# Kernel tuning notes

Hardware: AMD Instinct MI355X
Metric: run time of the kernel (lower is better)

The kernel has to match this reference:

```python
import jax, jax.numpy as jnp
import numpy as np
import math

B, CIN, COUT, K, G, SD, H = 8, 512, 512, 3, 16, 512, 32
EPS = 1e-8


def _blur_kernel():
    k = jnp.array([1., 3., 3., 1.], dtype=jnp.float32)
    k = k[None, :] * k[:, None]
    k = k / k.sum()
    return k * 4.0  # upsample_factor ** 2


def setup_inputs() -> dict:
    key = jax.random.key(0)
    ks = jax.random.split(key, 10)
    return {
        "x": jax.random.normal(ks[0], (B, CIN, H, H), jnp.float32),
        "co": jax.random.uniform(ks[1], (1, CIN, CIN), jnp.float32),
        "style": jax.random.normal(ks[2], (B, 2 * SD), jnp.float32),
        "noise": jax.random.normal(ks[3], (B, 1, 2 * H, 2 * H), jnp.float32),
        "W": jax.random.normal(ks[4], (1, COUT, CIN, K, K), jnp.float32),
        "mb_w": jax.random.normal(ks[5], (G, SD), jnp.float32),
        "mb_b": jnp.ones((G,), jnp.float32),
        "mod_w": jax.random.normal(ks[6], (CIN, SD), jnp.float32),
        "mod_b": jnp.ones((CIN,), jnp.float32),
        "cluster": jax.random.normal(ks[7], (G, CIN), jnp.float32),
        "gate": -jnp.ones((1,), jnp.float32),
        "tmpr": -2.0 * jnp.ones((1,), jnp.float32),
        "noise_weight": jnp.zeros((1,), jnp.float32),
        "flr_bias": jnp.zeros((COUT,), jnp.float32),
    }


def _l2norm(x, axis):
    n = jnp.linalg.norm(x, axis=axis, keepdims=True)
    return x / jnp.maximum(n, 1e-12)


def reference(x, co, style, noise, W, mb_w, mb_b, mod_w, mod_b,
              cluster, gate, tmpr, noise_weight, flr_bias):
    scale = 1.0 / math.sqrt(CIN * K * K)   # GroupModulatedConv2d.scale
    lin_scale = 1.0 / math.sqrt(SD)        # EqualLinear scale (lr_mul=1)

    t = jax.nn.sigmoid(tmpr) * 5.0
    g = jax.nn.sigmoid(gate)
    S = jax.nn.sigmoid((co - g) * 50.0)                    # (1,Cin,Cin)
    cl = jax.nn.softmax(t * cluster, axis=0)               # (G,Cin)
    loss1 = jnp.sum((cl.T @ cl - jax.lax.stop_gradient(S)) ** 2)
    loss2 = jnp.sum((jnp.float32(CIN * CIN / G) - jnp.sum(S)) ** 2)
    grouped = jax.lax.stop_gradient(jnp.round(jax.nn.softmax(cl * 500.0, axis=0))) + 1e-6

    s1, s2 = style[:, :SD], style[:, SD:]
    style_base = (s1 @ (mb_w * lin_scale).T + mb_b)[:, :, None]   # (B,G,1)
    st = (s2 @ (mod_w * lin_scale).T + mod_b)[:, None, :]         # (B,1,Cin)
    tmp = _l2norm(grouped[None] * st, axis=2)                     # (B,G,Cin)
    st = jnp.sum(tmp * style_base, axis=1)                        # (B,Cin)

    w = scale * W * st[:, None, :, None, None]                    # (B,Cout,Cin,K,K)
    demod = jax.lax.rsqrt(jnp.sum(w * w, axis=(2, 3, 4)) + EPS)   # (B,Cout)
    w = w * demod[:, :, None, None, None]

    # conv_transpose2d(stride=2, pad=0, groups=B) == per-sample conv with
    # lhs_dilation=2, padding=K-1, spatially-flipped kernel.
    wf = w[:, :, :, ::-1, ::-1]

    def per_sample(xi, wi):  # xi (Cin,h,w), wi (Cout,Cin,K,K)
        return jax.lax.conv_general_dilated(
            xi[None], wi, window_strides=(1, 1),
            padding=((K - 1, K - 1), (K - 1, K - 1)), lhs_dilation=(2, 2),
            dimension_numbers=('NCHW', 'OIHW', 'NCHW'))[0]

    out = jax.vmap(per_sample)(x, wf)                             # (B,Cout,65,65)

    # Blur: upfirdn2d, pad=(1,1), depthwise 4x4 symmetric FIR kernel.
    bk = _blur_kernel()
    kdw = jnp.broadcast_to(bk[None, None], (COUT, 1, 4, 4))
    out = jax.lax.conv_general_dilated(
        out, kdw, (1, 1), ((1, 1), (1, 1)), feature_group_count=COUT,
        dimension_numbers=('NCHW', 'OIHW', 'NCHW'))                # (B,Cout,64,64)

    # Correlation of base weights (detached, fed to next layer as `co`).
    wflat = W.reshape(COUT, -1)
    wn = _l2norm(wflat, axis=1)
    co_out = jax.lax.stop_gradient((wn @ wn.T)[None])              # (1,Cout,Cout)

    # NoiseInjection + FusedLeakyReLU
    out = out + noise_weight * noise
    out = jax.nn.leaky_relu(out + flr_bias[None, :, None, None], 0.2) * math.sqrt(2.0)
    return out, co_out, loss1, loss2
```

## Files before the change

kernel.cpp:

```cpp
#include <hip/hip_runtime.h>
#include <hip/hip_bf16.h>

#define NB 8
#define LIN_SCALE 0.044194173824159216f
#define SCALE 0.014731391274719736f

typedef __attribute__((ext_vector_type(8))) short short8;
typedef __attribute__((ext_vector_type(4))) float floatx4;

static constexpr size_t O_XS   = 0;
static constexpr size_t O_OUT1 = 9469952;
static constexpr size_t O_WRT  = 44081152;
static constexpr size_t O_WB   = 48799744;
static constexpr size_t O_PG   = 53518336;
static constexpr size_t O_WSQ  = 61906944;
static constexpr size_t O_CL   = 62955520;
static constexpr size_t O_GR   = O_CL + 32768;
static constexpr size_t O_SB   = O_GR + 32768;
static constexpr size_t O_ST0  = O_SB + 1024;
static constexpr size_t O_STS  = O_ST0 + 16384;
static constexpr size_t O_ST2  = O_STS + 16384;
static constexpr size_t O_WNI  = O_ST2 + 16384;
static constexpr size_t O_DM   = O_WNI + 2048;
static constexpr size_t O_ACC  = O_DM + 16384;

static constexpr size_t OUT_CO = 16777216;
static constexpr size_t OUT_L  = 17039360;

__device__ const int c_ylim[4] = {33,33,32,32};
__device__ const int c_xlim[4] = {33,32,33,32};
__device__ const int c_ntap[4] = {4,2,2,1};
__device__ const int c_tap0[4] = {0,4,6,8};
__device__ const int c_nmb[4]  = {69,66,66,64};
__device__ const int c_cnt[4]  = {276,264,264,256};
__device__ const int c_dy[9] = {-1,-1,0,0, -1,0, 0,0, 0};
__device__ const int c_dx[9] = {-1,0,-1,0, 0,0, -1,0, 0};
__device__ const int c_ky[9] = {2,2,0,0, 2,0, 1,1, 1};
__device__ const int c_kx[9] = {2,0,2,0, 1,1, 2,0, 1};
__device__ const long c_poff[4] = {0, 4460544, 8785920, 13111296};

__device__ __forceinline__ float wave_red(float v) {
#pragma unroll
  for (int s = 32; s > 0; s >>= 1) v += __shfl_down(v, s);
  return v;
}

__device__ __forceinline__ void gl_lds16(const void* g, void* l) {
  __builtin_amdgcn_global_load_lds((const __attribute__((address_space(1))) void*)g,
                                   (__attribute__((address_space(3))) void*)l, 16, 0, 0);
}

__device__ __forceinline__ unsigned short bf16b(float f) {
  union { __hip_bfloat16 h; unsigned short u; } cv;
  cv.h = __float2bfloat16(f);
  return cv.u;
}

__device__ __forceinline__ float bfu(unsigned short u) {
  union { float f; unsigned u32; } c; c.u32 = ((unsigned)u) << 16; return c.f;
}

__device__ __forceinline__ int xcd_chunk(int lb, int cnt) {
  const int q = cnt >> 3, r = cnt & 7;
  const int c = lb & 7, i = lb >> 3;
  return (c < r) ? c*(q+1) + i : r*(q+1) + (c - r)*q + i;
}

__global__ __launch_bounds__(256) void k_big1(const float* __restrict__ W,
    float* __restrict__ wsq, float* __restrict__ wni,
    __hip_bfloat16* __restrict__ wrt, unsigned short* __restrict__ wb,
    const float* __restrict__ style, const float* __restrict__ mod_w,
    const float* __restrict__ mod_b, float* __restrict__ st0,
    const float* __restrict__ co, const float* __restrict__ gate,
    const float* __restrict__ cluster, const float* __restrict__ tmpr,
    const float* __restrict__ mb_w, const float* __restrict__ mb_b,
    float* __restrict__ gr, float* __restrict__ sb,
    float* __restrict__ pacc, __hip_bfloat16* __restrict__ xs) {
  __shared__ float sh[8192];
  __shared__ float extra[8];
  const int bid = blockIdx.x, tid = threadIdx.x;
  const int lane = tid & 63, wv = tid >> 6;
  if (bid < 512) {
    const int o = bid;
    for (int j = tid; j < 4608; j += 256) sh[j] = W[(size_t)o*4608 + j];
    __syncthreads();
    float tot = 0.f;
#pragma unroll
    for (int half = 0; half < 2; half++) {
      const int i = tid + half*256;
      float s = 0.f;
#pragma unroll
      for (int k = 0; k < 9; k++) { float w = sh[i*9 + k]; s = fmaf(w, w, s); }
      wsq[o*512 + i] = s; tot += s;
#pragma unroll
      for (int tp = 0; tp < 9; tp++)
        wrt[((size_t)tp*512 + o)*512 + i] = __float2bfloat16(sh[i*9 + c_ky[tp]*3 + c_kx[tp]]);
    }
    for (int j = tid; j < 4608; j += 256) wb[(size_t)o*4608 + j] = bf16b(sh[j]);
    tot = wave_red(tot);
    if (lane == 0) extra[wv] = tot;
    __syncthreads();
    if (tid == 0) wni[o] = 1.f / fmaxf(sqrtf(extra[0]+extra[1]+extra[2]+extra[3]), 1e-12f);
  } else if (bid < 576) {
    const int b = (bid - 512) >> 3, oc = (bid - 512) & 7;
    sh[tid] = style[b*1024 + 512 + tid];
    sh[tid + 256] = style[b*1024 + 768 + tid];
    __syncthreads();
#pragma unroll
    for (int rr = 0; rr < 16; rr++) {
      const int c = oc*64 + wv*16 + rr;
      const float* mw = mod_w + (size_t)c*512;
      float acc = 0.f;
#pragma unroll
      for (int it = 0; it < 8; it++) acc = fmaf(mw[lane + 64*it], sh[lane + 64*it], acc);
      acc = wave_red(acc);
      if (lane == 0) st0[b*512 + c] = acc*LIN_SCALE + mod_b[c];
    }
  } else if (bid < 1088) {
    const int i = bid - 576;
    const float tt = 5.f / (1.f + expf(-tmpr[0]));
    const float gg = 1.f / (1.f + expf(-gate[0]));
    for (int j = tid; j < 512; j += 256) {
      float v[16]; float m = -1e30f;
#pragma unroll
      for (int g = 0; g < 16; g++) { v[g] = tt * cluster[g*512 + j]; m = fmaxf(m, v[g]); }
      float s = 0.f;
#pragma unroll
      for (int g = 0; g < 16; g++) { v[g] = expf(v[g] - m); s += v[g]; }
      float inv = 1.f / s;
#pragma unroll
      for (int g = 0; g < 16; g++) sh[g*512 + j] = v[g] * inv;
    }
    __syncthreads();
    float cli[16];
#pragma unroll
    for (int k = 0; k < 16; k++) cli[k] = sh[k*512 + i];
    float p1 = 0.f, p2 = 0.f;
    for (int j = tid; j < 512; j += 256) {
      float d = 0.f;
#pragma unroll
      for (int k = 0; k < 16; k++) d = fmaf(cli[k], sh[k*512 + j], d);
      float S = 1.f / (1.f + expf(-50.f*(co[i*512 + j] - gg)));
      float e = d - S;
      p1 = fmaf(e, e, p1); p2 += S;
    }
    p1 = wave_red(p1); p2 = wave_red(p2);
    if (lane == 0) { extra[wv] = p1; extra[4 + wv] = p2; }
    __syncthreads();
    if (tid == 0)  pacc[i]       = extra[0]+extra[1]+extra[2]+extra[3];
    if (tid == 64) pacc[512 + i] = extra[4]+extra[5]+extra[6]+extra[7];
  } else if (bid == 1088) {
    const float tt = 5.f / (1.f + expf(-tmpr[0]));
#pragma unroll
    for (int h = 0; h < 2; h++) {
      const int c = tid + h*256;
      float v[16]; float m = -1e30f;
#pragma unroll
      for (int g = 0; g < 16; g++) { v[g] = tt * cluster[g*512 + c]; m = fmaxf(m, v[g]); }
      float s = 0.f;
#pragma unroll
      for (int g = 0; g < 16; g++) { v[g] = expf(v[g] - m); s += v[g]; }
      float inv = 1.f / s;
      float clv[16]; float m2 = -1e30f;
#pragma unroll
      for (int g = 0; g < 16; g++) { clv[g] = v[g]*inv; m2 = fmaxf(m2, 500.f*clv[g]); }
      float s2 = 0.f; float e2[16];
#pragma unroll
      for (int g = 0; g < 16; g++) { e2[g] = expf(500.f*clv[g] - m2); s2 += e2[g]; }
      float i2 = 1.f / s2;
#pragma unroll
      for (int g = 0; g < 16; g++) gr[g*512 + c] = rintf(e2[g]*i2) + 1e-6f;
    }
    for (int task = wv; task < 128; task += 4) {
      int b = task >> 4, g = task & 15;
      const float* s1 = style + b*1024;
      const float* mw = mb_w + g*512;
      float acc = 0.f;
#pragma unroll
      for (int it = 0; it < 8; it++) acc = fmaf(s1[lane + 64*it], mw[lane + 64*it], acc);
      acc = wave_red(acc);
      if (lane == 0) sb[b*16 + g] = acc*LIN_SCALE + mb_b[g];
    }
  } else {
    const int id0 = (bid - 1089)*256 + tid;
    const float4 z = make_float4(0.f, 0.f, 0.f, 0.f);
    float4* xq = (float4*)xs;
#pragma unroll
    for (int it = 0; it < 22; ++it) {
      const int id = id0 + it*3072;
      const int c = id & 63;
      const int pb = id >> 6;
      const int b = pb / 132;
      const int pix = pb - b*132;
      int y, xx;
      if (pix < 34)       { y = 0;        xx = pix; }
      else if (pix < 68)  { y = 33;       xx = pix - 34; }
      else if (pix < 100) { y = pix - 67; xx = 0; }
      else                { y = pix - 99; xx = 33; }
      xq[((size_t)(b*34 + y)*34 + xx)*64 + c] = z;
    }
  }
}

__global__ __launch_bounds__(256) void k_mix(const float* __restrict__ st0,
    const float* __restrict__ gr, const float* __restrict__ sb,
    float* __restrict__ sts, float* __restrict__ st2,
    const float* __restrict__ pacc, float* __restrict__ out_tail) {
  if (blockIdx.x == 8) {
    const int tid = threadIdx.x;
    const int lane = tid & 63, wv = tid >> 6;
    __shared__ float r1[4], r2[4];
    float a = pacc[tid] + pacc[tid + 256];
    float b = pacc[512 + tid] + pacc[768 + tid];
    a = wave_red(a); b = wave_red(b);
    if (lane == 0) { r1[wv] = a; r2[wv] = b; }
    __syncthreads();
    if (tid == 0) {
      float p1 = r1[0]+r1[1]+r1[2]+r1[3];
      float p2 = r2[0]+r2[1]+r2[2]+r2[3];
      out_tail[0] = p1;
      float d = 16384.f - p2;
      out_tail[1] = d*d;
    }
    return;
  }
  const int b = blockIdx.x, tid = threadIdx.x;
  const int lane = tid & 63, wv = tid >> 6;
  float s0 = st0[b*512 + tid], s1 = st0[b*512 + 256 + tid];
  float g0[16], g1[16];
#pragma unroll
  for (int g = 0; g < 16; g++) { g0[g] = gr[g*512 + tid]; g1[g] = gr[g*512 + 256 + tid]; }
  __shared__ float red[16][4];
  __shared__ float inv[16];
  __shared__ float sbb[16];
#pragma unroll
  for (int g = 0; g < 16; g++) {
    float a = g0[g]*s0, c = g1[g]*s1;
    float p = wave_red(a*a + c*c);
    if (lane == 0) red[g][wv] = p;
  }
  if (tid < 16) sbb[tid] = sb[b*16 + tid];
  __syncthreads();
  if (tid < 16) {
    float tt = red[tid][0] + red[tid][1] + red[tid][2] + red[tid][3];
    inv[tid] = 1.f / fmaxf(sqrtf(tt), 1e-12f);
  }
  __syncthreads();
  float f0 = 0.f, f1 = 0.f;
#pragma unroll
  for (int g = 0; g < 16; g++) {
    float w = inv[g]*sbb[g];
    f0 = fmaf(g0[g], w, f0); f1 = fmaf(g1[g], w, f1);
  }
  float sn0 = s0*f0, sn1 = s1*f1;
  sts[b*512 + tid] = sn0*SCALE;        st2[b*512 + tid] = sn0*sn0;
  sts[b*512 + 256 + tid] = sn1*SCALE;  st2[b*512 + 256 + tid] = sn1*sn1;
}

__global__ __launch_bounds__(256) void k_big2(const float* __restrict__ st2,
    const float* __restrict__ wsq, float* __restrict__ dm,
    const float* __restrict__ x, const float* __restrict__ sts,
    __hip_bfloat16* __restrict__ xs) {
  __shared__ float L[64*65];
  const int tid = threadIdx.x;
  const int lane = tid & 63, wv = tid >> 6;
  if (blockIdx.x < 64) {
    const int b = blockIdx.x >> 3, oc = blockIdx.x & 7;
    L[tid] = st2[b*512 + tid];
    L[tid + 256] = st2[b*512 + 256 + tid];
    __syncthreads();
#pragma unroll
    for (int rr = 0; rr < 16; rr++) {
      const int o = oc*64 + wv*16 + rr;
      const float* wp = wsq + (size_t)o*512;
      float acc = 0.f;
#pragma unroll
      for (int it = 0; it < 8; it++) acc = fmaf(wp[lane + 64*it], L[lane + 64*it], acc);
      acc = wave_red(acc);
      if (lane == 0) dm[b*512 + o] = rsqrtf((1.0f/4608.0f)*acc + 1e-8f);
    }
    return;
  }
  const int id = blockIdx.x - 64;
  const int b = id >> 7;
  const int p0 = ((id >> 3) & 15) * 64;
  const int i0 = (id & 7) * 64;
  const int lp = tid & 63, li = tid >> 6;
  const float* xp = x + ((size_t)b*512 + i0)*1024 + p0;
#pragma unroll
  for (int ii = 0; ii < 16; ii++) {
    const int i = li + 4*ii;
    L[i*65 + lp] = xp[(size_t)i*1024 + lp];
  }
  __syncthreads();
  const int iw = tid & 63, pw = tid >> 6;
  const float sv = sts[b*512 + i0 + iw];
#pragma unroll
  for (int pp = 0; pp < 16; pp++) {
    const int pix = p0 + pw + 4*pp;
    const int y = pix >> 5, xq = pix & 31;
    xs[(((size_t)b*34 + (y+1))*34 + (xq+1))*512 + i0 + iw] = __float2bfloat16(L[iw*65 + pw + 4*pp] * sv);
  }
}

__global__ __launch_bounds__(256, 4) void k_mfma(
    const __hip_bfloat16* __restrict__ xs, const __hip_bfloat16* __restrict__ wrt,
    __hip_bfloat16* __restrict__ out1, const __hip_bfloat16* __restrict__ wb,
    float* __restrict__ pgram) {
  __shared__ __hip_bfloat16 smem[8704];
  const int fid = blockIdx.x;
  const int tid = threadIdx.x;
  const int lane = tid & 63, wv = tid >> 6;
  const int wm = (wv >> 1) << 6, wn = (wv & 1) << 6;
  const int col16 = lane & 15, quad = lane >> 4;
  const int colp = col16 ^ ((col16 >> 2) & 1);
  const int soff = (quad ^ (col16 & 3)) << 3;

  int aoff[4], boff[4];
#pragma unroll
  for (int t = 0; t < 4; t++) {
    aoff[t] = (wm + t*16 + colp)*32 + soff;
    boff[t] = 4096 + (wn + t*16 + colp)*32 + soff;
  }
  floatx4 acc[4][4];
#pragma unroll
  for (int i = 0; i < 4; i++)
#pragma unroll
    for (int j = 0; j < 4; j++) acc[i][j] = (floatx4){0.f, 0.f, 0.f, 0.f};

  if (fid >= 276 && fid < 404) {
    const int g = xcd_chunk(fid - 276, 128);
    const int m0 = (g & 3) * 128, n0 = ((g >> 2) & 3) * 128;
    const long kz = (long)(g >> 4) * 576;
    long abase[2], bbase[2]; int ldso[2];
#pragma unroll
    for (int r = 0; r < 2; r++) {
      const int idx = r*256 + tid;
      const int rowp = idx >> 2;
      const int row = rowp ^ ((rowp >> 2) & 1);
      const int kc = (((idx & 3) ^ (row & 3)) << 3);
      abase[r] = (long)(m0 + row)*4608 + kz + kc;
      bbase[r] = (long)(n0 + row)*4608 + kz + kc;
      ldso[r] = idx << 3;
    }
    for (int ks = 0; ks < 18; ks++) {
      const int kk = ks << 5;
#pragma unroll
      for (int r = 0; r < 2; r++) {
        gl_lds16(wb + (abase[r] + kk), smem + ldso[r]);
        gl_lds16(wb + (bbase[r] + kk), smem + 4096 + ldso[r]);
      }
      __syncthreads();
      short8 af[4], bf[4];
#pragma unroll
      for (int t = 0; t < 4; t++) {
        af[t] = *(const short8*)(smem + aoff[t]);
        bf[t] = *(const short8*)(smem + boff[t]);
      }
#pragma unroll
      for (int i = 0; i < 4; i++)
#pragma unroll
        for (int j = 0; j < 4; j++)
          acc[i][j] = __builtin_amdgcn_mfma_f32_16x16x32_bf16(af[i], bf[j], acc[i][j], 0, 0, 0);
      __syncthreads();
    }
    float* pg = pgram + (size_t)(g >> 4) * 262144;
#pragma unroll
    for (int i = 0; i < 4; i++)
#pragma unroll
      for (int j = 0; j < 4; j++) {
        const int m = m0 + wm + i*16 + (quad << 2);
        const int n = n0 + wn + j*16 + col16;
#pragma unroll
        for (int r = 0; r < 4; r++) pg[(size_t)(m + r)*512 + n] = acc[i][j][r];
      }
    return;
  }

  int cls, lb;
  if (fid < 276)      { cls = 0; lb = fid; }
  else if (fid < 668) { cls = 1; lb = fid - 404; }
  else if (fid < 932) { cls = 2; lb = fid - 668; }
  else                { cls = 3; lb = fid - 932; }
  const int lg = xcd_chunk(lb, c_cnt[cls]);
  const int mb = lg >> 2, nb = lg & 3;
  const int xlim = c_xlim[cls];
  const int npix = c_ylim[cls] * xlim;
  const int M = NB * npix;
  const int m0 = mb * 128, n0 = nb * 128;
  const int t0 = c_tap0[cls];
  const int ntap = c_ntap[cls];

  long abase[2], bbase[2]; int ldso[2];
#pragma unroll
  for (int r = 0; r < 2; r++) {
    const int idx = r*256 + tid;
    const int rowp = idx >> 2;
    const int row = rowp ^ ((rowp >> 2) & 1);
    const int kc = (((idx & 3) ^ (row & 3)) << 3);
    int rm = m0 + row; if (rm >= M) rm = 0;
    const int b = rm / npix; const int rem = rm - b*npix;
    const int yy = rem / xlim; const int xx = rem - yy*xlim;
    abase[r] = ((long)(b*34 + yy + 1)*34 + (xx + 1))*512 + kc;
    bbase[r] = ((long)(t0*512 + n0 + row))*512 + kc;
    ldso[r] = idx << 3;
  }

  for (int tp = 0; tp < ntap; tp++) {
    const int tap = t0 + tp;
    const long adel = (long)((c_dy[tap]*34 + c_dx[tap])*512);
    const long bdel = (long)tp << 18;
    for (int ks = 0; ks < 16; ks++) {
      const int kk = ks << 5;
#pragma unroll
      for (int r = 0; r < 2; r++) {
        gl_lds16(xs + (abase[r] + adel + kk), smem + ldso[r]);
        gl_lds16(wrt + (bbase[r] + bdel + kk), smem + 4096 + ldso[r]);
      }
      __syncthreads();
      short8 af[4], bf[4];
#pragma unroll
      for (int t = 0; t < 4; t++) {
        af[t] = *(const short8*)(smem + aoff[t]);
        bf[t] = *(const short8*)(smem + boff[t]);
      }
#pragma unroll
      for (int i = 0; i < 4; i++)
#pragma unroll
        for (int j = 0; j < 4; j++)
          acc[i][j] = __builtin_amdgcn_mfma_f32_16x16x32_bf16(af[i], bf[j], acc[i][j], 0, 0, 0);
      __syncthreads();
    }
  }

  __hip_bfloat16* plane = out1 + c_poff[cls];
#pragma unroll
  for (int h = 0; h < 2; h++) {
    if ((wv & 1) == h) {
#pragma unroll
      for (int i = 0; i < 4; i++) {
        const int mrow = wm + i*16 + (quad << 2);
#pragma unroll
        for (int j = 0; j < 4; j++) {
          const int ncl = j*16 + col16;
          ushort4 v;
          v.x = bf16b(acc[i][j][0]); v.y = bf16b(acc[i][j][1]);
          v.z = bf16b(acc[i][j][2]); v.w = bf16b(acc[i][j][3]);
          *(ushort4*)(smem + ncl*136 + mrow) = v;
        }
      }
    }
    __syncthreads();
#pragma unroll
    for (int it = 0; it < 4; it++) {
      const int c = it*256 + tid;
      const int ol = c >> 4, ml = (c & 15) << 3;
      const int mg = m0 + ml;
      if (mg < M) {
        const ushort4 v = *(const ushort4*)(smem + ol*136 + ml);
        *(ushort4*)(plane + (long)(n0 + h*64 + ol)*M + mg) = v;
      }
    }
    __syncthreads();
  }
}

__global__ __launch_bounds__(256) void k_blur(const __hip_bfloat16* __restrict__ out1,
    const float* __restrict__ dm, const float* __restrict__ noise,
    const float* __restrict__ nw, const float* __restrict__ fb, float* __restrict__ out,
    const float* __restrict__ pgram, const float* __restrict__ wni,
    float* __restrict__ co_out) {
  if (blockIdx.x < 256) {
    const int i4 = blockIdx.x*256 + threadIdx.x;
    float4 s = make_float4(0.f, 0.f, 0.f, 0.f);
#pragma unroll
    for (int z = 0; z < 8; z++) {
      const float4 v = ((const float4*)(pgram + (size_t)z*262144))[i4];
      s.x += v.x; s.y += v.y; s.z += v.z; s.w += v.w;
    }
    const float wm = wni[i4 >> 7];
    const float4 wn4 = ((const float4*)wni)[i4 & 127];
    float4 o;
    o.x = s.x*wm*wn4.x; o.y = s.y*wm*wn4.y; o.z = s.z*wm*wn4.z; o.w = s.w*wm*wn4.w;
    ((float4*)co_out)[i4] = o;
    return;
  }
  const int bo = blockIdx.x - 256;
  const int b = bo >> 9, o = bo & 511;
  __shared__ unsigned short L[65 * 68];
  const int tid = threadIdx.x;
  const unsigned short* p0 = (const unsigned short*)out1 + 0        + (long)o * 8712 + b * 1089;
  const unsigned short* p1 = (const unsigned short*)out1 + 4460544  + (long)o * 8448 + b * 1056;
  const unsigned short* p2 = (const unsigned short*)out1 + 8785920  + (long)o * 8448 + b * 1056;
  const unsigned short* p3 = (const unsigned short*)out1 + 13111296 + (long)o * 8192 + b * 1024;
  for (int m = tid; m < 65; m += 256) { L[m*68 + 0] = 0; L[m*68 + 66] = 0; }
  for (int e = tid; e < 1089; e += 256) { int y = e / 33, x = e - 33*y; L[(2*y)*68 + 2*x + 1] = p0[e]; }
  for (int e = tid; e < 1056; e += 256) { int y = e >> 5, x = e & 31;   L[(2*y)*68 + 2*x + 2] = p1[e]; }
  for (int e = tid; e < 1056; e += 256) { int y = e / 33, x = e - 33*y; L[(2*y+1)*68 + 2*x + 1] = p2[e]; }
  for (int e = tid; e < 1024; e += 256) { int y = e >> 5, x = e & 31;   L[(2*y+1)*68 + 2*x + 2] = p3[e]; }
  __syncthreads();
  const float dmv = dm[bo];
  const float nwv = nw[0];
  const float bv = fb[o];
  const int Q = tid & 63;
  const int qy = tid >> 6;
  const int mbase = 16 * qy - 1;
  float hs[18];
#pragma unroll
  for (int rm = 0; rm < 18; rm++) {
    const int m = mbase + rm;
    float s = 0.f;
    if (m >= 0 && m <= 64) {
      const unsigned short* row = L + m*68 + Q;
      s = 0.25f * (bfu(row[0]) + bfu(row[3])) + 0.75f * (bfu(row[1]) + bfu(row[2]));
    }
    hs[rm] = s;
  }
  float* op = out + ((size_t)bo << 12);
  const float* npl = noise + ((size_t)b << 12);
#pragma unroll
  for (int pp = 0; pp < 16; pp++) {
    const int P = 16 * qy + pp;
    float s = 0.25f * (hs[pp] + hs[pp + 3]) + 0.75f * (hs[pp + 1] + hs[pp + 2]);
    float v = fmaf(dmv, s, fmaf(nwv, npl[P * 64 + Q], bv));
    v = (v >= 0.f ? v : 0.2f * v) * 1.4142135623730951f;
    op[P * 64 + Q] = v;
  }
}

extern "C" void kernel_launch(void* const* d_in, const int* in_sizes, int n_in,
                              void* d_out, int out_size, void* d_ws, size_t ws_size,
                              hipStream_t stream) {
  const float* x       = (const float*)d_in[0];
  const float* co      = (const float*)d_in[1];
  const float* style   = (const float*)d_in[2];
  const float* noise   = (const float*)d_in[3];
  const float* W       = (const float*)d_in[4];
  const float* mb_w    = (const float*)d_in[5];
  const float* mb_b    = (const float*)d_in[6];
  const float* mod_w   = (const float*)d_in[7];
  const float* mod_b   = (const float*)d_in[8];
  const float* cluster = (const float*)d_in[9];
  const float* gate    = (const float*)d_in[10];
  const float* tmpr    = (const float*)d_in[11];
  const float* nw      = (const float*)d_in[12];
  const float* fb      = (const float*)d_in[13];
  float* out = (float*)d_out;
  char* ws = (char*)d_ws;

  __hip_bfloat16* xs   = (__hip_bfloat16*)(ws + O_XS);
  __hip_bfloat16* out1 = (__hip_bfloat16*)(ws + O_OUT1);
  __hip_bfloat16* wrt  = (__hip_bfloat16*)(ws + O_WRT);
  __hip_bfloat16* wb   = (__hip_bfloat16*)(ws + O_WB);
  float* pgram = (float*)(ws + O_PG);
  float* wsq = (float*)(ws + O_WSQ);
  float* gr  = (float*)(ws + O_GR);
  float* sb  = (float*)(ws + O_SB);
  float* st0 = (float*)(ws + O_ST0);
  float* sts = (float*)(ws + O_STS);
  float* st2 = (float*)(ws + O_ST2);
  float* wni = (float*)(ws + O_WNI);
  float* dm  = (float*)(ws + O_DM);
  float* pacc = pgram;

  k_big1<<<1101, 256, 0, stream>>>(W, wsq, wni, wrt, (unsigned short*)wb,
                                   style, mod_w, mod_b, st0, co, gate,
                                   cluster, tmpr, mb_w, mb_b, gr, sb, pacc, xs);
  k_mix<<<9, 256, 0, stream>>>(st0, gr, sb, sts, st2, pacc, out + OUT_L);
  k_big2<<<1088, 256, 0, stream>>>(st2, wsq, dm, x, sts, xs);
  k_mfma<<<1188, 256, 0, stream>>>(xs, wrt, out1, wb, pgram);
  k_blur<<<4352, 256, 0, stream>>>(out1, dm, noise, nw, fb, out, pgram, wni, out + OUT_CO);
}
```

Before: 256.1 us.

## Double-buffer MFMA LDS stages and fold style mixing into prep kernel

The main MFMA conv and gram loops now use two LDS buffers. The next k-slice's global-to-LDS loads are issued before computing the current one, with manual vmcnt waits and barriers replacing the two __syncthreads per step. Separately, the small k_mix kernel is removed. Each k_big2 block recomputes its sample's style normalisation inline, and the loss tail moves to an extra block, which saves one launch and its intermediate buffers. LDS per block doubles, which may lower occupancy under launch_bounds(256,4), and every k_big2 block now does redundant style work.

```diff
diff --git a/kernel.cpp b/kernel.cpp
--- a/kernel.cpp
+++ b/kernel.cpp
@@ -202,37 +202,39 @@
   }
 }
 
-__global__ __launch_bounds__(256) void k_mix(const float* __restrict__ st0,
+__global__ __launch_bounds__(256) void k_big2(const float* __restrict__ st0,
     const float* __restrict__ gr, const float* __restrict__ sb,
-    float* __restrict__ sts, float* __restrict__ st2,
+    const float* __restrict__ wsq, float* __restrict__ dm,
+    const float* __restrict__ x, __hip_bfloat16* __restrict__ xs,
     const float* __restrict__ pacc, float* __restrict__ out_tail) {
-  if (blockIdx.x == 8) {
-    const int tid = threadIdx.x;
-    const int lane = tid & 63, wv = tid >> 6;
-    __shared__ float r1[4], r2[4];
+  __shared__ float L[64*65];
+  __shared__ float red[16][4];
+  __shared__ float inv[16];
+  __shared__ float sbb[16];
+  const int tid = threadIdx.x;
+  const int lane = tid & 63, wv = tid >> 6;
+
+  if (blockIdx.x == 1088) {
     float a = pacc[tid] + pacc[tid + 256];
-    float b = pacc[512 + tid] + pacc[768 + tid];
-    a = wave_red(a); b = wave_red(b);
-    if (lane == 0) { r1[wv] = a; r2[wv] = b; }
+    float b2 = pacc[512 + tid] + pacc[768 + tid];
+    a = wave_red(a); b2 = wave_red(b2);
+    if (lane == 0) { red[0][wv] = a; red[1][wv] = b2; }
     __syncthreads();
     if (tid == 0) {
-      float p1 = r1[0]+r1[1]+r1[2]+r1[3];
-      float p2 = r2[0]+r2[1]+r2[2]+r2[3];
+      float p1 = red[0][0]+red[0][1]+red[0][2]+red[0][3];
+      float p2 = red[1][0]+red[1][1]+red[1][2]+red[1][3];
       out_tail[0] = p1;
       float d = 16384.f - p2;
       out_tail[1] = d*d;
     }
     return;
   }
-  const int b = blockIdx.x, tid = threadIdx.x;
-  const int lane = tid & 63, wv = tid >> 6;
+
+  const int b = (blockIdx.x < 64) ? (blockIdx.x >> 3) : ((blockIdx.x - 64) >> 7);
   float s0 = st0[b*512 + tid], s1 = st0[b*512 + 256 + tid];
   float g0[16], g1[16];
 #pragma unroll
   for (int g = 0; g < 16; g++) { g0[g] = gr[g*512 + tid]; g1[g] = gr[g*512 + 256 + tid]; }
-  __shared__ float red[16][4];
-  __shared__ float inv[16];
-  __shared__ float sbb[16];
 #pragma unroll
   for (int g = 0; g < 16; g++) {
     float a = g0[g]*s0, c = g1[g]*s1;
@@ -242,8 +244,8 @@
   if (tid < 16) sbb[tid] = sb[b*16 + tid];
   __syncthreads();
   if (tid < 16) {
-    float tt = red[tid][0] + red[tid][1] + red[tid][2] + red[tid][3];
-    inv[tid] = 1.f / fmaxf(sqrtf(tt), 1e-12f);
+    float ttn = red[tid][0] + red[tid][1] + red[tid][2] + red[tid][3];
+    inv[tid] = 1.f / fmaxf(sqrtf(ttn), 1e-12f);
   }
   __syncthreads();
   float f0 = 0.f, f1 = 0.f;
@@ -252,22 +254,12 @@
     float w = inv[g]*sbb[g];
     f0 = fmaf(g0[g], w, f0); f1 = fmaf(g1[g], w, f1);
   }
-  float sn0 = s0*f0, sn1 = s1*f1;
-  sts[b*512 + tid] = sn0*SCALE;        st2[b*512 + tid] = sn0*sn0;
-  sts[b*512 + 256 + tid] = sn1*SCALE;  st2[b*512 + 256 + tid] = sn1*sn1;
-}
-
-__global__ __launch_bounds__(256) void k_big2(const float* __restrict__ st2,
-    const float* __restrict__ wsq, float* __restrict__ dm,
-    const float* __restrict__ x, const float* __restrict__ sts,
-    __hip_bfloat16* __restrict__ xs) {
-  __shared__ float L[64*65];
-  const int tid = threadIdx.x;
-  const int lane = tid & 63, wv = tid >> 6;
+  const float sn0 = s0*f0, sn1 = s1*f1;
+
   if (blockIdx.x < 64) {
-    const int b = blockIdx.x >> 3, oc = blockIdx.x & 7;
-    L[tid] = st2[b*512 + tid];
-    L[tid + 256] = st2[b*512 + 256 + tid];
+    const int oc = blockIdx.x & 7;
+    L[tid] = sn0*sn0;
+    L[tid + 256] = sn1*sn1;
     __syncthreads();
 #pragma unroll
     for (int rr = 0; rr < 16; rr++) {
@@ -281,10 +273,16 @@
     }
     return;
   }
+
+  L[tid] = sn0*SCALE;
+  L[tid + 256] = sn1*SCALE;
+  __syncthreads();
   const int id = blockIdx.x - 64;
-  const int b = id >> 7;
   const int p0 = ((id >> 3) & 15) * 64;
   const int i0 = (id & 7) * 64;
+  const int iw = tid & 63, pw = tid >> 6;
+  const float sv = L[i0 + iw];
+  __syncthreads();
   const int lp = tid & 63, li = tid >> 6;
   const float* xp = x + ((size_t)b*512 + i0)*1024 + p0;
 #pragma unroll
@@ -293,8 +291,6 @@
     L[i*65 + lp] = xp[(size_t)i*1024 + lp];
   }
   __syncthreads();
-  const int iw = tid & 63, pw = tid >> 6;
-  const float sv = sts[b*512 + i0 + iw];
 #pragma unroll
   for (int pp = 0; pp < 16; pp++) {
     const int pix = p0 + pw + 4*pp;
@@ -307,7 +303,7 @@
     const __hip_bfloat16* __restrict__ xs, const __hip_bfloat16* __restrict__ wrt,
     __hip_bfloat16* __restrict__ out1, const __hip_bfloat16* __restrict__ wb,
     float* __restrict__ pgram) {
-  __shared__ __hip_bfloat16 smem[8704];
+  __shared__ __hip_bfloat16 smem[16384];
   const int fid = blockIdx.x;
   const int tid = threadIdx.x;
   const int lane = tid & 63, wv = tid >> 6;
@@ -343,26 +339,35 @@
       bbase[r] = (long)(n0 + row)*4608 + kz + kc;
       ldso[r] = idx << 3;
     }
-    for (int ks = 0; ks < 18; ks++) {
-      const int kk = ks << 5;
-#pragma unroll
-      for (int r = 0; r < 2; r++) {
-        gl_lds16(wb + (abase[r] + kk), smem + ldso[r]);
-        gl_lds16(wb + (bbase[r] + kk), smem + 4096 + ldso[r]);
+#define STAGE_GRAM(s_) do { \
+      const int kk_ = (s_) << 5; \
+      const int lo_ = ((s_) & 1) << 13; \
+      gl_lds16(wb + (abase[0] + kk_), smem + lo_ + ldso[0]); \
+      gl_lds16(wb + (abase[1] + kk_), smem + lo_ + ldso[1]); \
+      gl_lds16(wb + (bbase[0] + kk_), smem + lo_ + 4096 + ldso[0]); \
+      gl_lds16(wb + (bbase[1] + kk_), smem + lo_ + 4096 + ldso[1]); \
+    } while (0)
+    STAGE_GRAM(0);
+    for (int s = 0; s < 18; ++s) {
+      if (s + 1 < 18) {
+        STAGE_GRAM(s + 1);
+        asm volatile("s_waitcnt vmcnt(4)\n\ts_barrier" ::: "memory");
+      } else {
+        asm volatile("s_waitcnt vmcnt(0)\n\ts_barrier" ::: "memory");
       }
-      __syncthreads();
-      short8 af[4], bf[4];
+      const int lo = (s & 1) << 13;
+      short8 af[4], bfr[4];
 #pragma unroll
       for (int t = 0; t < 4; t++) {
-        af[t] = *(const short8*)(smem + aoff[t]);
-        bf[t] = *(const short8*)(smem + boff[t]);
+        af[t]  = *(const short8*)(smem + lo + aoff[t]);
+        bfr[t] = *(const short8*)(smem + lo + boff[t]);
       }
 #pragma unroll
       for (int i = 0; i < 4; i++)
 #pragma unroll
         for (int j = 0; j < 4; j++)
-          acc[i][j] = __builtin_amdgcn_mfma_f32_16x16x32_bf16(af[i], bf[j], acc[i][j], 0, 0, 0);
-      __syncthreads();
+          acc[i][j] = __builtin_amdgcn_mfma_f32_16x16x32_bf16(af[i], bfr[j], acc[i][j], 0, 0, 0);
+      asm volatile("s_barrier" ::: "memory");
     }
     float* pg = pgram + (size_t)(g >> 4) * 262144;
 #pragma unroll
@@ -406,31 +411,39 @@
     ldso[r] = idx << 3;
   }
 
-  for (int tp = 0; tp < ntap; tp++) {
-    const int tap = t0 + tp;
-    const long adel = (long)((c_dy[tap]*34 + c_dx[tap])*512);
-    const long bdel = (long)tp << 18;
-    for (int ks = 0; ks < 16; ks++) {
-      const int kk = ks << 5;
-#pragma unroll
-      for (int r = 0; r < 2; r++) {
-        gl_lds16(xs + (abase[r] + adel + kk), smem + ldso[r]);
-        gl_lds16(wrt + (bbase[r] + bdel + kk), smem + 4096 + ldso[r]);
-      }
-      __syncthreads();
-      short8 af[4], bf[4];
-#pragma unroll
-      for (int t = 0; t < 4; t++) {
-        af[t] = *(const short8*)(smem + aoff[t]);
-        bf[t] = *(const short8*)(smem + boff[t]);
-      }
-#pragma unroll
-      for (int i = 0; i < 4; i++)
-#pragma unroll
-        for (int j = 0; j < 4; j++)
-          acc[i][j] = __builtin_amdgcn_mfma_f32_16x16x32_bf16(af[i], bf[j], acc[i][j], 0, 0, 0);
-      __syncthreads();
-    }
+  const int nst = ntap << 4;
+#define STAGE_CONV(s_) do { \
+    const int tap_ = t0 + ((s_) >> 4); \
+    const long adel_ = (long)((c_dy[tap_]*34 + c_dx[tap_])*512); \
+    const long bdel_ = (long)((s_) >> 4) << 18; \
+    const int kk_ = ((s_) & 15) << 5; \
+    const int lo_ = ((s_) & 1) << 13; \
+    gl_lds16(xs + (abase[0] + adel_ + kk_), smem + lo_ + ldso[0]); \
+    gl_lds16(xs + (abase[1] + adel_ + kk_), smem + lo_ + ldso[1]); \
+    gl_lds16(wrt + (bbase[0] + bdel_ + kk_), smem + lo_ + 4096 + ldso[0]); \
+    gl_lds16(wrt + (bbase[1] + bdel_ + kk_), smem + lo_ + 4096 + ldso[1]); \
+  } while (0)
+  STAGE_CONV(0);
+  for (int s = 0; s < nst; ++s) {
+    if (s + 1 < nst) {
+      STAGE_CONV(s + 1);
+      asm volatile("s_waitcnt vmcnt(4)\n\ts_barrier" ::: "memory");
+    } else {
+      asm volatile("s_waitcnt vmcnt(0)\n\ts_barrier" ::: "memory");
+    }
+    const int lo = (s & 1) << 13;
+    short8 af[4], bfr[4];
+#pragma unroll
+    for (int t = 0; t < 4; t++) {
+      af[t]  = *(const short8*)(smem + lo + aoff[t]);
+      bfr[t] = *(const short8*)(smem + lo + boff[t]);
+    }
+#pragma unroll
+    for (int i = 0; i < 4; i++)
+#pragma unroll
+      for (int j = 0; j < 4; j++)
+        acc[i][j] = __builtin_amdgcn_mfma_f32_16x16x32_bf16(af[i], bfr[j], acc[i][j], 0, 0, 0);
+    asm volatile("s_barrier" ::: "memory");
   }
 
   __hip_bfloat16* plane = out1 + c_poff[cls];
@@ -557,17 +570,14 @@
   float* gr  = (float*)(ws + O_GR);
   float* sb  = (float*)(ws + O_SB);
   float* st0 = (float*)(ws + O_ST0);
-  float* sts = (float*)(ws + O_STS);
-  float* st2 = (float*)(ws + O_ST2);
   float* wni = (float*)(ws + O_WNI);
   float* dm  = (float*)(ws + O_DM);
-  float* pacc = pgram;
+  float* pacc = (float*)(ws + O_STS);
 
   k_big1<<<1101, 256, 0, stream>>>(W, wsq, wni, wrt, (unsigned short*)wb,
                                    style, mod_w, mod_b, st0, co, gate,
                                    cluster, tmpr, mb_w, mb_b, gr, sb, pacc, xs);
-  k_mix<<<9, 256, 0, stream>>>(st0, gr, sb, sts, st2, pacc, out + OUT_L);
-  k_big2<<<1088, 256, 0, stream>>>(st2, wsq, dm, x, sts, xs);
+  k_big2<<<1089, 256, 0, stream>>>(st0, gr, sb, wsq, dm, x, xs, pacc, out + OUT_L);
   k_mfma<<<1188, 256, 0, stream>>>(xs, wrt, out1, wb, pgram);
   k_blur<<<4352, 256, 0, stream>>>(out1, dm, noise, nw, fb, out, pgram, wni, out + OUT_CO);
 }
```

Measured after the change: 241.4 us. 1.06x faster.
